# Optimization experiments

Measured on AMD Instinct MI355X. Metric: run time of the kernel, lower is better.

## Reference

```python
import jax, jax.numpy as jnp
import numpy as np

B, S, D, H = 2, 2048, 1024, 16
DK = D // H
WINDOW = 256


def _make_mask():
    # causal local-window sparsity: attend to j in (i-WINDOW, i]
    i = np.arange(S)[:, None]
    j = np.arange(S)[None, :]
    m = (j <= i) & (i - j < WINDOW)
    return jnp.asarray(m)


def setup_inputs() -> dict:
    key = jax.random.key(0)
    ks = jax.random.split(key, 9)
    sw = 1.0 / np.sqrt(D)
    return {
        "x": jax.random.normal(ks[0], (B, S, D), dtype=jnp.float32),
        "wq": jax.random.normal(ks[1], (D, D), dtype=jnp.float32) * sw,
        "bq": jnp.zeros((D,), dtype=jnp.float32),
        "wk": jax.random.normal(ks[2], (D, D), dtype=jnp.float32) * sw,
        "bk": jnp.zeros((D,), dtype=jnp.float32),
        "wv": jax.random.normal(ks[3], (D, D), dtype=jnp.float32) * sw,
        "bv": jnp.zeros((D,), dtype=jnp.float32),
        "wo": jax.random.normal(ks[4], (D, D), dtype=jnp.float32) * sw,
        "bo": jnp.zeros((D,), dtype=jnp.float32),
        "mask": _make_mask(),
    }


def reference(x, wq, bq, wk, bk, wv, bv, wo, bo, mask):
    b, s, d = x.shape
    # projections (torch Linear: x @ W.T + b), split heads -> [b, h, s, dk]
    def proj(w, bias):
        return (x @ w.T + bias).reshape(b, s, H, DK).transpose(0, 2, 1, 3)

    q = proj(wq, bq)
    k = proj(wk, bk)
    v = proj(wv, bv)

    scores = jnp.einsum("bhqd,bhkd->bhqk", q, k) / jnp.sqrt(jnp.float32(DK))
    scores = jnp.where(mask, scores, -jnp.inf)  # mask broadcasts over b, h
    attn = jax.nn.softmax(scores, axis=-1)
    out = jnp.einsum("bhqk,bhkd->bhqd", attn, v)
    out = out.transpose(0, 2, 1, 3).reshape(b, s, d)
    return out @ wo.T + bo
```

## Files before the change

kernel.cpp:

```cpp
#include <hip/hip_runtime.h>

#define S_LEN 2048
#define DMODEL 1024
#define NHEADS 16
#define WIN 256

typedef unsigned short u16;
typedef unsigned int u32;
typedef __attribute__((ext_vector_type(8))) __bf16 bf16x8;
typedef __attribute__((ext_vector_type(4))) float f32x4;
typedef __attribute__((ext_vector_type(8))) u16 u16x8;
typedef __attribute__((ext_vector_type(4))) u16 u16x4;

__device__ __forceinline__ u16 f2bf(float f) {
  u32 u = __builtin_bit_cast(u32, f);
  u += 0x7fffu + ((u >> 16) & 1u);
  return (u16)(u >> 16);
}

#define GLDS16(g, l) __builtin_amdgcn_global_load_lds( \
    (const __attribute__((address_space(1))) void*)(g), \
    (__attribute__((address_space(3))) void*)(l), 16, 0, 0)

__global__ __launch_bounds__(256) void cast_all(
    const float* __restrict__ x, const float* __restrict__ wq, const float* __restrict__ wk,
    const float* __restrict__ wv, const float* __restrict__ wo,
    u16* __restrict__ xb, u16* __restrict__ wqb, u16* __restrict__ wkb,
    u16* __restrict__ wvb, u16* __restrict__ wob) {
  const int e = (blockIdx.x * 256 + threadIdx.x) * 4;
  const float* src; u16* dst; int off;
  if (e < (1 << 22)) { src = x; dst = xb; off = e; }
  else {
    int r = e - (1 << 22);
    int seg = r >> 20; off = r & ((1 << 20) - 1);
    src = (seg == 0) ? wq : (seg == 1) ? wk : (seg == 2) ? wv : wo;
    dst = (seg == 0) ? wqb : (seg == 1) ? wkb : (seg == 2) ? wvb : wob;
  }
  float4 v = *(const float4*)(src + off);
  u16x4 o = { f2bf(v.x), f2bf(v.y), f2bf(v.z), f2bf(v.w) };
  *(u16x4*)(dst + off) = o;
}

__global__ __launch_bounds__(256) void gemm_nt(
    const u16* __restrict__ A,
    const u16* __restrict__ B0, const u16* __restrict__ B1, const u16* __restrict__ B2,
    const float* __restrict__ bias0, const float* __restrict__ bias1, const float* __restrict__ bias2,
    u16* __restrict__ C0, u16* __restrict__ C1, u16* __restrict__ C2,
    const int M, const int N, const int K)
{
  const u16* Bt; const float* bias; u16* C;
  if (blockIdx.z == 0)      { Bt = B0; bias = bias0; C = C0; }
  else if (blockIdx.z == 1) { Bt = B1; bias = bias1; C = C1; }
  else                      { Bt = B2; bias = bias2; C = C2; }

  __shared__ u16 As[2][128 * 32];
  __shared__ u16 Bs[2][128 * 32];

  const int t = threadIdx.x;
  const int row0 = blockIdx.x * 128;
  const int col0 = blockIdx.y * 128;
  const int lane = t & 63, lo = lane & 15, hi = lane >> 4;
  const int wv = t >> 6;
  const int wr = (wv >> 1) * 64, wc = (wv & 1) * 64;

  f32x4 acc[4][4];
  #pragma unroll
  for (int i = 0; i < 4; ++i)
    #pragma unroll
    for (int j = 0; j < 4; ++j) acc[i][j] = (f32x4)0.0f;

  const int NT = K >> 5;

  auto stage = [&](int buf, int kt) {
    const int kof = kt * 32;
    #pragma unroll
    for (int c = 0; c < 2; ++c) {
      const int off = t * 16 + c * 4096;
      const int r = off >> 6;
      const int ke = (off & 63) >> 1;
      GLDS16(A  + (size_t)(row0 + r) * K + (kof + ke), (u16*)As + buf * (128 * 32) + (off >> 1));
      GLDS16(Bt + (size_t)(col0 + r) * K + (kof + ke), (u16*)Bs + buf * (128 * 32) + (off >> 1));
    }
  };

  stage(0, 0);
  int cur = 0;
  for (int kt = 0; kt < NT; ++kt) {
    __syncthreads();
    if (kt + 1 < NT) stage(cur ^ 1, kt + 1);
    bf16x8 af[4], bfr[4];
    #pragma unroll
    for (int mi = 0; mi < 4; ++mi)
      af[mi] = *(const bf16x8*)&As[cur][(wr + mi * 16 + lo) * 32 + hi * 8];
    #pragma unroll
    for (int ni = 0; ni < 4; ++ni)
      bfr[ni] = *(const bf16x8*)&Bs[cur][(wc + ni * 16 + lo) * 32 + hi * 8];
    #pragma unroll
    for (int mi = 0; mi < 4; ++mi)
      #pragma unroll
      for (int ni = 0; ni < 4; ++ni)
        acc[mi][ni] = __builtin_amdgcn_mfma_f32_16x16x32_bf16(af[mi], bfr[ni], acc[mi][ni], 0, 0, 0);
    cur ^= 1;
  }

  #pragma unroll
  for (int mi = 0; mi < 4; ++mi) {
    #pragma unroll
    for (int ni = 0; ni < 4; ++ni) {
      const int col = col0 + wc + ni * 16 + lo;
      const float bv = bias[col];
      #pragma unroll
      for (int r = 0; r < 4; ++r) {
        const int row = row0 + wr + mi * 16 + hi * 4 + r;
        C[(size_t)row * N + col] = f2bf(acc[mi][ni][r] + bv);
      }
    }
  }
}

__global__ __launch_bounds__(256) void gemm_out64(
    const u16* __restrict__ A, const u16* __restrict__ Bt,
    const float* __restrict__ bias, float* __restrict__ C)
{
  constexpr int N = 1024, K = 1024;

  __shared__ u16 As[2][128 * 32];
  __shared__ u16 Bs[2][64 * 32];

  int id = blockIdx.y * gridDim.x + blockIdx.x;
  int wgid = (id & 7) * 64 + (id >> 3);
  const int row0 = (wgid >> 4) * 128;
  const int col0 = (wgid & 15) * 64;

  const int t = threadIdx.x;
  const int lane = t & 63, lo = lane & 15, hi = lane >> 4;
  const int wv = t >> 6;
  const int wr = (wv >> 1) * 64, wc = (wv & 1) * 32;

  f32x4 acc[4][2];
  #pragma unroll
  for (int i = 0; i < 4; ++i)
    #pragma unroll
    for (int j = 0; j < 2; ++j) acc[i][j] = (f32x4)0.0f;

  auto stage = [&](int buf, int kt) {
    const int kof = kt * 32;
    #pragma unroll
    for (int c = 0; c < 2; ++c) {
      const int off = t * 16 + c * 4096;
      const int r = off >> 6;
      const int ke = (off & 63) >> 1;
      GLDS16(A + (size_t)(row0 + r) * K + (kof + ke), (u16*)As + buf * (128 * 32) + (off >> 1));
    }
    {
      const int off = t * 16;
      const int r = off >> 6;
      const int ke = (off & 63) >> 1;
      GLDS16(Bt + (size_t)(col0 + r) * K + (kof + ke), (u16*)Bs + buf * (64 * 32) + (off >> 1));
    }
  };

  stage(0, 0);
  int cur = 0;
  for (int kt = 0; kt < (K >> 5); ++kt) {
    __syncthreads();
    if (kt + 1 < (K >> 5)) stage(cur ^ 1, kt + 1);
    bf16x8 af[4], bfr[2];
    #pragma unroll
    for (int mi = 0; mi < 4; ++mi)
      af[mi] = *(const bf16x8*)&As[cur][(wr + mi * 16 + lo) * 32 + hi * 8];
    #pragma unroll
    for (int ni = 0; ni < 2; ++ni)
      bfr[ni] = *(const bf16x8*)&Bs[cur][(wc + ni * 16 + lo) * 32 + hi * 8];
    #pragma unroll
    for (int mi = 0; mi < 4; ++mi)
      #pragma unroll
      for (int ni = 0; ni < 2; ++ni)
        acc[mi][ni] = __builtin_amdgcn_mfma_f32_16x16x32_bf16(af[mi], bfr[ni], acc[mi][ni], 0, 0, 0);
    cur ^= 1;
  }

  #pragma unroll
  for (int mi = 0; mi < 4; ++mi) {
    #pragma unroll
    for (int ni = 0; ni < 2; ++ni) {
      const int col = col0 + wc + ni * 16 + lo;
      const float bv = bias[col];
      #pragma unroll
      for (int r = 0; r < 4; ++r) {
        const int row = row0 + wr + mi * 16 + hi * 4 + r;
        C[(size_t)row * N + col] = acc[mi][ni][r] + bv;
      }
    }
  }
}

__device__ __forceinline__ int swz(int row, int col) {
  int byte = (row << 7) + (col << 1);
  byte ^= (row & 7) << 4;
  return byte >> 1;
}

__global__ __launch_bounds__(256) void attn_win(const u16* __restrict__ Q,
                                                const u16* __restrict__ K,
                                                const u16* __restrict__ V,
                                                u16* __restrict__ O) {
  const int qt = blockIdx.x, h = blockIdx.y, b = blockIdx.z;
  const int q0 = qt * 64;
  const int t = threadIdx.x;
  const int wv = t >> 6, lane = t & 63, lo = lane & 15, hi = lane >> 4;

  __shared__ u16 Qs[64 * 64];
  __shared__ u16 Ks[64 * 64];
  __shared__ u16 Vt[64 * 64];
  __shared__ u16 Ps[4][16 * 64];

  const size_t base = ((size_t)b * S_LEN) * DMODEL + h * 64;

  #pragma unroll
  for (int c = 0; c < 2; ++c) {
    const int off = t * 16 + c * 4096;
    const int r = off >> 7, ce = (off & 127) >> 1;
    GLDS16(Q + base + (size_t)(q0 + r) * DMODEL + ce, (u16*)Qs + (off >> 1));
  }
  __syncthreads();

  bf16x8 qf[2];
  #pragma unroll
  for (int kq = 0; kq < 2; ++kq)
    qf[kq] = *(const bf16x8*)&Qs[(wv * 16 + lo) * 64 + kq * 32 + hi * 8];

  f32x4 oacc[4];
  #pragma unroll
  for (int i = 0; i < 4; ++i) oacc[i] = (f32x4)0.0f;
  float m_r[4] = {-1e30f, -1e30f, -1e30f, -1e30f};
  float l_r[4] = {0.f, 0.f, 0.f, 0.f};

  const int vrow = t >> 2;
  const int vc0  = (t & 3) * 16;

  for (int kt = 0; kt < 5; ++kt) {
    const int kstart = q0 - 256 + kt * 64;
    if (kstart + 63 < 0) continue;
    __syncthreads();

    {
      const int jg = kstart + vrow;
      if (jg >= 0) {
        const u16* srcK = K + base + (size_t)jg * DMODEL + vc0;
        u16x8 k0 = *(const u16x8*)(srcK);
        u16x8 k1 = *(const u16x8*)(srcK + 8);
        *(u16x8*)&Ks[swz(vrow, vc0)]     = k0;
        *(u16x8*)&Ks[swz(vrow, vc0 + 8)] = k1;
        const u16* srcV = V + base + (size_t)jg * DMODEL + vc0;
        u16x8 v0 = *(const u16x8*)(srcV);
        u16x8 v1 = *(const u16x8*)(srcV + 8);
        #pragma unroll
        for (int e = 0; e < 8; ++e) {
          Vt[swz(vc0 + e, vrow)]     = v0[e];
          Vt[swz(vc0 + 8 + e, vrow)] = v1[e];
        }
      } else {
        u16x8 z = (u16x8)0;
        *(u16x8*)&Ks[swz(vrow, vc0)]     = z;
        *(u16x8*)&Ks[swz(vrow, vc0 + 8)] = z;
        #pragma unroll
        for (int e = 0; e < 16; ++e) Vt[swz(vc0 + e, vrow)] = 0;
      }
    }
    __syncthreads();

    f32x4 sfr[4];
    #pragma unroll
    for (int ni = 0; ni < 4; ++ni) {
      sfr[ni] = (f32x4)0.0f;
      #pragma unroll
      for (int kq = 0; kq < 2; ++kq) {
        bf16x8 kf = *(const bf16x8*)&Ks[swz(ni * 16 + lo, kq * 32 + hi * 8)];
        sfr[ni] = __builtin_amdgcn_mfma_f32_16x16x32_bf16(qf[kq], kf, sfr[ni], 0, 0, 0);
      }
    }

    float sv[4][4], cmax[4] = {-1e30f, -1e30f, -1e30f, -1e30f};
    const int i0 = q0 + wv * 16 + hi * 4;
    #pragma unroll
    for (int ni = 0; ni < 4; ++ni) {
      const int j = kstart + ni * 16 + lo;
      #pragma unroll
      for (int r = 0; r < 4; ++r) {
        const int i = i0 + r;
        float x = sfr[ni][r] * 0.125f;
        const bool ok = (j >= 0) & (j <= i) & (i - j < WIN);
        x = ok ? x : -1e30f;
        sv[ni][r] = x;
        cmax[r] = fmaxf(cmax[r], x);
      }
    }
    #pragma unroll
    for (int d = 1; d < 16; d <<= 1) {
      #pragma unroll
      for (int r = 0; r < 4; ++r) cmax[r] = fmaxf(cmax[r], __shfl_xor(cmax[r], d));
    }

    float pr[4][4], rsum[4];
    #pragma unroll
    for (int r = 0; r < 4; ++r) {
      const float mnew = fmaxf(m_r[r], cmax[r]);
      const float sc = __expf(m_r[r] - mnew);
      m_r[r] = mnew;
      l_r[r] *= sc;
      #pragma unroll
      for (int ni = 0; ni < 4; ++ni) oacc[ni][r] *= sc;
      float s = 0.f;
      #pragma unroll
      for (int ni = 0; ni < 4; ++ni) {
        const float p = __expf(sv[ni][r] - mnew);
        pr[ni][r] = p;
        s += p;
      }
      rsum[r] = s;
    }
    #pragma unroll
    for (int d = 1; d < 16; d <<= 1) {
      #pragma unroll
      for (int r = 0; r < 4; ++r) rsum[r] += __shfl_xor(rsum[r], d);
    }
    #pragma unroll
    for (int r = 0; r < 4; ++r) l_r[r] += rsum[r];

    #pragma unroll
    for (int ni = 0; ni < 4; ++ni)
      #pragma unroll
      for (int r = 0; r < 4; ++r)
        Ps[wv][swz(hi * 4 + r, ni * 16 + lo)] = f2bf(pr[ni][r]);

    bf16x8 pa[2];
    #pragma unroll
    for (int kp = 0; kp < 2; ++kp)
      pa[kp] = *(const bf16x8*)&Ps[wv][swz(lo, kp * 32 + hi * 8)];
    #pragma unroll
    for (int ni = 0; ni < 4; ++ni) {
      #pragma unroll
      for (int kp = 0; kp < 2; ++kp) {
        bf16x8 vf = *(const bf16x8*)&Vt[swz(ni * 16 + lo, kp * 32 + hi * 8)];
        oacc[ni] = __builtin_amdgcn_mfma_f32_16x16x32_bf16(pa[kp], vf, oacc[ni], 0, 0, 0);
      }
    }
  }

  #pragma unroll
  for (int ni = 0; ni < 4; ++ni) {
    #pragma unroll
    for (int r = 0; r < 4; ++r) {
      const int row = q0 + wv * 16 + hi * 4 + r;
      O[base + (size_t)row * DMODEL + ni * 16 + lo] = f2bf(oacc[ni][r] / l_r[r]);
    }
  }
}

extern "C" void kernel_launch(void* const* d_in, const int* in_sizes, int n_in,
                              void* d_out, int out_size, void* d_ws, size_t ws_size,
                              hipStream_t stream) {
  const float* x  = (const float*)d_in[0];
  const float* wq = (const float*)d_in[1];
  const float* bq = (const float*)d_in[2];
  const float* wk = (const float*)d_in[3];
  const float* bk = (const float*)d_in[4];
  const float* wvp = (const float*)d_in[5];
  const float* bv = (const float*)d_in[6];
  const float* wo = (const float*)d_in[7];
  const float* bo = (const float*)d_in[8];
  float* out = (float*)d_out;

  char* ws = (char*)d_ws;
  const size_t MB = 1024 * 1024;
  u16* xb  = (u16*)(ws);
  u16* wqb = (u16*)(ws + 8 * MB);
  u16* wkb = (u16*)(ws + 10 * MB);
  u16* wvb = (u16*)(ws + 12 * MB);
  u16* wob = (u16*)(ws + 14 * MB);
  u16* Qb  = (u16*)(ws + 16 * MB);
  u16* Kb  = (u16*)(ws + 24 * MB);
  u16* Vb  = (u16*)(ws + 32 * MB);
  u16* Ob  = (u16*)(ws + 40 * MB);

  cast_all<<<8192, 256, 0, stream>>>(x, wq, wk, wvp, wo, xb, wqb, wkb, wvb, wob);

  dim3 g1(4096 / 128, 1024 / 128, 3);
  gemm_nt<<<g1, 256, 0, stream>>>(xb, wqb, wkb, wvb, bq, bk, bv,
                                  Qb, Kb, Vb, 4096, 1024, 1024);

  attn_win<<<dim3(S_LEN / 64, NHEADS, 2), 256, 0, stream>>>(Qb, Kb, Vb, Ob);

  gemm_out64<<<dim3(32, 16), 256, 0, stream>>>(Ob, wob, bo, out);
}
```

Baseline: 95.94 us.

## Double-buffer K/V tiles with register prefetch and reswizzle V transpose

Turns the attention kernel's K/V tile loading into a register-prefetch double-buffer pipeline. The next tile's global loads are issued before the current tile's MFMAs, then written into the alternate LDS buffer afterwards. This removes one barrier per iteration and overlaps load latency with compute. It also adds a second XOR term to the transposed-V swizzle to cut LDS bank conflicts on the scalar transpose stores. The costs are double the LDS for K/V and extra registers held across the compute phase.

```diff
diff --git a/kernel.cpp b/kernel.cpp
--- a/kernel.cpp
+++ b/kernel.cpp
@@ -195,9 +195,14 @@
   }
 }
 
-__device__ __forceinline__ int swz(int row, int col) {
+__device__ __forceinline__ int swzK(int row, int col) {
   int byte = (row << 7) + (col << 1);
   byte ^= (row & 7) << 4;
+  return byte >> 1;
+}
+__device__ __forceinline__ int swzV(int d, int j) {
+  int byte = (d << 7) + (j << 1);
+  byte ^= ((d & 7) << 4) ^ (((d >> 4) & 3) << 5);
   return byte >> 1;
 }
 
@@ -211,8 +216,8 @@
   const int wv = t >> 6, lane = t & 63, lo = lane & 15, hi = lane >> 4;
 
   __shared__ u16 Qs[64 * 64];
-  __shared__ u16 Ks[64 * 64];
-  __shared__ u16 Vt[64 * 64];
+  __shared__ u16 Ks[2][64 * 64];
+  __shared__ u16 Vt[2][64 * 64];
   __shared__ u16 Ps[4][16 * 64];
 
   const size_t base = ((size_t)b * S_LEN) * DMODEL + h * 64;
@@ -223,6 +228,35 @@
     const int r = off >> 7, ce = (off & 127) >> 1;
     GLDS16(Q + base + (size_t)(q0 + r) * DMODEL + ce, (u16*)Qs + (off >> 1));
   }
+
+  const int vrow = t >> 2;
+  const int vc0  = (t & 3) * 16;
+  const int ktmin = max(0, (256 - q0) >> 6);
+
+  u16x8 kra, krb, vra, vrb;
+  auto issue = [&](int kt) {
+    const int jg = q0 - 256 + kt * 64 + vrow;
+    if (jg >= 0) {
+      const u16* sk = K + base + (size_t)jg * DMODEL + vc0;
+      kra = *(const u16x8*)sk; krb = *(const u16x8*)(sk + 8);
+      const u16* sv = V + base + (size_t)jg * DMODEL + vc0;
+      vra = *(const u16x8*)sv; vrb = *(const u16x8*)(sv + 8);
+    } else {
+      kra = (u16x8)0; krb = (u16x8)0; vra = (u16x8)0; vrb = (u16x8)0;
+    }
+  };
+  auto commit = [&](int buf) {
+    *(u16x8*)&Ks[buf][swzK(vrow, vc0)]     = kra;
+    *(u16x8*)&Ks[buf][swzK(vrow, vc0 + 8)] = krb;
+    #pragma unroll
+    for (int e = 0; e < 8; ++e) {
+      Vt[buf][swzV(vc0 + e, vrow)]     = vra[e];
+      Vt[buf][swzV(vc0 + 8 + e, vrow)] = vrb[e];
+    }
+  };
+
+  issue(ktmin);
+  commit(0);
   __syncthreads();
 
   bf16x8 qf[2];
@@ -236,39 +270,10 @@
   float m_r[4] = {-1e30f, -1e30f, -1e30f, -1e30f};
   float l_r[4] = {0.f, 0.f, 0.f, 0.f};
 
-  const int vrow = t >> 2;
-  const int vc0  = (t & 3) * 16;
-
-  for (int kt = 0; kt < 5; ++kt) {
+  int cur = 0;
+  for (int kt = ktmin; kt < 5; ++kt) {
     const int kstart = q0 - 256 + kt * 64;
-    if (kstart + 63 < 0) continue;
-    __syncthreads();
-
-    {
-      const int jg = kstart + vrow;
-      if (jg >= 0) {
-        const u16* srcK = K + base + (size_t)jg * DMODEL + vc0;
-        u16x8 k0 = *(const u16x8*)(srcK);
-        u16x8 k1 = *(const u16x8*)(srcK + 8);
-        *(u16x8*)&Ks[swz(vrow, vc0)]     = k0;
-        *(u16x8*)&Ks[swz(vrow, vc0 + 8)] = k1;
-        const u16* srcV = V + base + (size_t)jg * DMODEL + vc0;
-        u16x8 v0 = *(const u16x8*)(srcV);
-        u16x8 v1 = *(const u16x8*)(srcV + 8);
-        #pragma unroll
-        for (int e = 0; e < 8; ++e) {
-          Vt[swz(vc0 + e, vrow)]     = v0[e];
-          Vt[swz(vc0 + 8 + e, vrow)] = v1[e];
-        }
-      } else {
-        u16x8 z = (u16x8)0;
-        *(u16x8*)&Ks[swz(vrow, vc0)]     = z;
-        *(u16x8*)&Ks[swz(vrow, vc0 + 8)] = z;
-        #pragma unroll
-        for (int e = 0; e < 16; ++e) Vt[swz(vc0 + e, vrow)] = 0;
-      }
-    }
-    __syncthreads();
+    if (kt < 4) issue(kt + 1);
 
     f32x4 sfr[4];
     #pragma unroll
@@ -276,7 +281,7 @@
       sfr[ni] = (f32x4)0.0f;
       #pragma unroll
       for (int kq = 0; kq < 2; ++kq) {
-        bf16x8 kf = *(const bf16x8*)&Ks[swz(ni * 16 + lo, kq * 32 + hi * 8)];
+        bf16x8 kf = *(const bf16x8*)&Ks[cur][swzK(ni * 16 + lo, kq * 32 + hi * 8)];
         sfr[ni] = __builtin_amdgcn_mfma_f32_16x16x32_bf16(qf[kq], kf, sfr[ni], 0, 0, 0);
       }
     }
@@ -332,20 +337,25 @@
     for (int ni = 0; ni < 4; ++ni)
       #pragma unroll
       for (int r = 0; r < 4; ++r)
-        Ps[wv][swz(hi * 4 + r, ni * 16 + lo)] = f2bf(pr[ni][r]);
+        Ps[wv][swzK(hi * 4 + r, ni * 16 + lo)] = f2bf(pr[ni][r]);
 
     bf16x8 pa[2];
     #pragma unroll
     for (int kp = 0; kp < 2; ++kp)
-      pa[kp] = *(const bf16x8*)&Ps[wv][swz(lo, kp * 32 + hi * 8)];
+      pa[kp] = *(const bf16x8*)&Ps[wv][swzK(lo, kp * 32 + hi * 8)];
+
     #pragma unroll
     for (int ni = 0; ni < 4; ++ni) {
       #pragma unroll
       for (int kp = 0; kp < 2; ++kp) {
-        bf16x8 vf = *(const bf16x8*)&Vt[swz(ni * 16 + lo, kp * 32 + hi * 8)];
+        bf16x8 vf = *(const bf16x8*)&Vt[cur][swzV(ni * 16 + lo, kp * 32 + hi * 8)];
         oacc[ni] = __builtin_amdgcn_mfma_f32_16x16x32_bf16(pa[kp], vf, oacc[ni], 0, 0, 0);
       }
     }
+
+    if (kt < 4) commit(cur ^ 1);
+    __syncthreads();
+    cur ^= 1;
   }
 
   #pragma unroll
```

New measurement: 94.71 us. No clear change (-1.3%).
